# Performance work log

Measured on AMD Instinct MI355X. Metric: run time of the kernel, lower is better.

The kernel has to match this reference:

```python
import jax, jax.numpy as jnp
import numpy as np

LPB = 0.03   # lower_probability_bound
LEB = 0.2    # lower_entropy_bound
UEB = 0.5    # upper_entropy_bound
BETA = 1.0
N, K, S, D = 8192, 1000, 8, 1024


def setup_inputs() -> dict:
    key = jax.random.key(0)
    k1, k2, k3 = jax.random.split(key, 3)
    x = jax.random.normal(k1, (N, D), dtype=jnp.float32)
    # per-sample logit temperature so entropies spread across the gating band
    base = jax.random.normal(k2, (N, K), dtype=jnp.float32)
    scales = jax.random.uniform(k3, (N, 1), dtype=jnp.float32, minval=1.0, maxval=15.0)
    text_logits = base * scales
    memory = jnp.zeros((K, S, D), dtype=jnp.float32)
    # init_entropy(prop_max=1): -log(1/K) = log(K)
    memory_entropy = jnp.full((K, S), jnp.log(jnp.float32(K)), dtype=jnp.float32)
    memory_state = jnp.zeros((K, S), dtype=bool)
    return {"x": x, "text_logits": text_logits, "memory": memory,
            "memory_entropy": memory_entropy, "memory_state": memory_state}


def _update_memory(memory, memory_entropy, memory_state, x, text_logits):
    """Sequential entropy-gated scatter update (order-dependent, as in torch loop)."""
    def step(carry, inp):
        mem, ent, st = carry
        xi, li = inp                      # xi: [D], li: [K]
        p = jax.nn.softmax(li)
        lab = jnp.argmax(li)
        H = -jnp.sum(jnp.log(p + 1e-6) * p)  # shannon entropy
        row = ent[lab]                    # [S] entropies of this class's slots
        cond = (p[lab] > LPB) & (H > LEB) & (H < UEB) & jnp.any(H < row)
        idx = jnp.argmax(row)             # evict highest-entropy slot
        mem = mem.at[lab, idx].set(jnp.where(cond, xi, mem[lab, idx]))
        ent = ent.at[lab, idx].set(jnp.where(cond, H, ent[lab, idx]))
        st = st.at[lab, idx].set(jnp.where(cond, True, st[lab, idx]))
        return (mem, ent, st), cond

    (mem, ent, st), selected = jax.lax.scan(
        step, (memory, memory_entropy, memory_state), (x, text_logits))
    return mem, ent, st, selected


def reference(x, text_logits, memory, memory_entropy, memory_state):
    mem, ent, st, selected = _update_memory(memory, memory_entropy, memory_state, x, text_logits)
    # get_logits: A_ = (memory @ x.T).permute(2,0,1) -> [N, K, S]
    A_ = jnp.einsum('ksd,nd->nks', mem, x)
    logits = -jnp.sum(jnp.exp(-BETA * (1.0 - A_)), axis=-1)  # [N, K]
    return logits
```

## Files before the change

### kernel.cpp

```cpp
#include <hip/hip_runtime.h>
#include <hip/hip_bf16.h>
#include <math.h>

#define NN 8192
#define KK 1000
#define SS 8
#define DD 1024
#define RR (KK * SS)
#define RRP 8192

typedef __bf16 bf16x8 __attribute__((ext_vector_type(8)));
typedef float f32x4 __attribute__((ext_vector_type(4)));
typedef unsigned short ushort_t;
typedef ushort_t ushort8 __attribute__((ext_vector_type(8)));

static __device__ __forceinline__ ushort_t f2bf(float f) {
  unsigned u = __float_as_uint(f);
  unsigned r = (u + 0x7FFFu + ((u >> 16) & 1u)) >> 16;
  return (ushort_t)r;
}

#define GLD16(gsrc, ldst)                                                     \
  __builtin_amdgcn_global_load_lds(                                           \
      (const __attribute__((address_space(1))) unsigned int*)(gsrc),          \
      (__attribute__((address_space(3))) unsigned int*)(ldst), 16, 0, 0)

#define SBAR() asm volatile("s_barrier" ::: "memory")
#define WAITVM(n) asm volatile("s_waitcnt vmcnt(" #n ")" ::: "memory")

__global__ __launch_bounds__(256) void stats_kernel(
    const float* __restrict__ tl, int2* __restrict__ cand) {
  __shared__ float sv[KK];
  __shared__ float redv[256];
  __shared__ int   redi[256];
  const int n = blockIdx.x;
  const int t = threadIdx.x;
  const float* row = tl + (size_t)n * KK;
  for (int j = t; j < KK; j += 256) sv[j] = row[j];
  __syncthreads();

  float bv = -INFINITY; int bi = KK;
  for (int j = t; j < KK; j += 256) { float v = sv[j]; if (v > bv) { bv = v; bi = j; } }
  redv[t] = bv; redi[t] = bi;
  __syncthreads();
  for (int off = 128; off > 0; off >>= 1) {
    if (t < off) {
      float ov = redv[t + off]; int oi = redi[t + off];
      if (ov > redv[t] || (ov == redv[t] && oi < redi[t])) { redv[t] = ov; redi[t] = oi; }
    }
    __syncthreads();
  }
  const float m = redv[0];
  const int lab = redi[0];
  __syncthreads();

  float z = 0.f;
  for (int j = t; j < KK; j += 256) z += expf(sv[j] - m);
  redv[t] = z;
  __syncthreads();
  for (int off = 128; off > 0; off >>= 1) {
    if (t < off) redv[t] += redv[t + off];
    __syncthreads();
  }
  const float Z = redv[0];
  __syncthreads();

  float h = 0.f;
  for (int j = t; j < KK; j += 256) {
    float p = expf(sv[j] - m) / Z;
    h -= p * logf(p + 1e-6f);
  }
  redv[t] = h;
  __syncthreads();
  for (int off = 128; off > 0; off >>= 1) {
    if (t < off) redv[t] += redv[t + off];
    __syncthreads();
  }
  if (t == 0) {
    const float H = redv[0];
    const float plab = 1.0f / Z;
    const bool c = (plab > 0.03f) && (H > 0.2f) && (H < 0.5f);
    cand[n] = make_int2(c ? lab : -1, __float_as_int(H));
  }
}

__global__ __launch_bounds__(256) void select_kernel(
    const int2* __restrict__ cand, const float* __restrict__ ment,
    int* __restrict__ sel) {
  const int w = threadIdx.x >> 6;
  const int l = threadIdx.x & 63;
  const int k = blockIdx.x * 4 + w;
  if (k >= KK) return;

  float ent[SS]; int idx[SS];
  #pragma unroll
  for (int s = 0; s < SS; ++s) { ent[s] = ment[k * SS + s]; idx[s] = -1; }

  for (int base = 0; base < NN; base += 64) {
    const int2 c = cand[base + l];
    unsigned long long msk = __ballot(c.x == k);
    while (msk) {
      const int src = __ffsll((long long)msk) - 1;
      msk &= msk - 1;
      const float H = __shfl(__int_as_float(c.y), src);
      float mx = ent[0]; int mi = 0;
      #pragma unroll
      for (int s = 1; s < SS; ++s) if (ent[s] > mx) { mx = ent[s]; mi = s; }
      if (H < mx) { ent[mi] = H; idx[mi] = base + src; }
    }
  }
  if (l == 0) {
    #pragma unroll
    for (int s = 0; s < SS; ++s) sel[k * SS + s] = idx[s];
  }
}

__global__ __launch_bounds__(128) void convgather_kernel(
    const float* __restrict__ x, const float* __restrict__ mem,
    const int* __restrict__ sel, ushort_t* __restrict__ xb,
    ushort_t* __restrict__ Bb) {
  const int r = blockIdx.x;
  const int t = threadIdx.x;
  const float* src;
  ushort_t* dst;
  if (r < NN) {
    src = x + (size_t)r * DD;
    dst = xb + (size_t)r * DD;
  } else {
    const int rr = r - NN;
    dst = Bb + (size_t)rr * DD;
    if (rr >= RR) {
      *(ushort8*)(dst + t * 8) = (ushort8)0;
      return;
    }
    const int sl = sel[rr];
    src = (sl >= 0) ? (x + (size_t)sl * DD) : (mem + (size_t)rr * DD);
  }
  const float4 a = *(const float4*)(src + t * 8);
  const float4 b = *(const float4*)(src + t * 8 + 4);
  ushort8 o;
  o[0] = f2bf(a.x); o[1] = f2bf(a.y); o[2] = f2bf(a.z); o[3] = f2bf(a.w);
  o[4] = f2bf(b.x); o[5] = f2bf(b.y); o[6] = f2bf(b.z); o[7] = f2bf(b.w);
  *(ushort8*)(dst + t * 8) = o;
}

#define BKS 64
#define NTS (DD / BKS)
#define LDSH 32768

__global__ __launch_bounds__(512, 2) void logits_kernel(
    const ushort_t* __restrict__ xb, const ushort_t* __restrict__ Bb,
    float* __restrict__ out) {
  __shared__ ushort_t lds[2 * LDSH];
  const int t = threadIdx.x;
  const int w = t >> 6;
  const int l = t & 63;
  const int wm = w >> 2;
  const int wn = w & 3;
  const int n0 = blockIdx.x * 256;
  const int r0 = blockIdx.y * 256;

  const int srow = w * 8 + (l >> 3);
  const int gcolh = (((l & 7) ^ ((l >> 3) & 7)) << 3);
  const ushort_t* gA = xb + (size_t)(n0 + srow) * DD + gcolh;
  const ushort_t* gB = Bb + (size_t)(r0 + srow) * DD + gcolh;

#define STAGE_AC(T, c)                                                        \
  GLD16(gA + (size_t)(c) * 64 * DD + (size_t)(T) * BKS,                       \
        lds + ((T) & 1) * LDSH + (c) * 4096 + w * 512)
#define STAGE_BC(T, c)                                                        \
  GLD16(gB + (size_t)(c) * 64 * DD + (size_t)(T) * BKS,                       \
        lds + ((T) & 1) * LDSH + 16384 + (c) * 4096 + w * 512)

  const int lr = l & 15;
  const int ch = l >> 4;
  const int kc0 = ((ch ^ (lr & 7)) << 3);
  const int kc1 = (((4 + ch) ^ (lr & 7)) << 3);
  const int arow = (wm * 128 + lr) * 64;
  const int brow = 16384 + (wn * 64 + lr) * 64;

  f32x4 acc[8][4];
  #pragma unroll
  for (int mi = 0; mi < 8; ++mi)
    #pragma unroll
    for (int ni = 0; ni < 4; ++ni) acc[mi][ni] = (f32x4){0.f, 0.f, 0.f, 0.f};

  STAGE_AC(0, 0); STAGE_AC(0, 2);
  STAGE_BC(0, 0); STAGE_BC(0, 2);
  STAGE_BC(0, 1); STAGE_BC(0, 3);
  STAGE_AC(0, 1); STAGE_AC(0, 3);
  WAITVM(2);
  SBAR();

#define MFMA_CLUSTER(q)                                                       \
  do {                                                                        \
    __builtin_amdgcn_sched_barrier(0);                                        \
    __builtin_amdgcn_s_setprio(1);                                            \
    _Pragma("unroll")                                                         \
    for (int i = 0; i < 2; ++i)                                               \
      _Pragma("unroll")                                                       \
      for (int ni = 0; ni < 4; ++ni)                                          \
        acc[2 * (q) + i][ni] = __builtin_amdgcn_mfma_f32_16x16x32_bf16(       \
            af[i][0], bf[ni][0], acc[2 * (q) + i][ni], 0, 0, 0);              \
    _Pragma("unroll")                                                         \
    for (int i = 0; i < 2; ++i)                                               \
      _Pragma("unroll")                                                       \
      for (int ni = 0; ni < 4; ++ni)                                          \
        acc[2 * (q) + i][ni] = __builtin_amdgcn_mfma_f32_16x16x32_bf16(       \
            af[i][1], bf[ni][1], acc[2 * (q) + i][ni], 0, 0, 0);              \
    __builtin_amdgcn_s_setprio(0);                                            \
    __builtin_amdgcn_sched_barrier(0);                                        \
  } while (0)

  #pragma unroll 2
  for (int T = 0; T < NTS; ++T) {
    const ushort_t* buf = lds + (T & 1) * LDSH;
    const int Tn = T + 1;
    const bool st = (Tn < NTS);
    bf16x8 bf[4][2];
    bf16x8 af[2][2];

    #pragma unroll
    for (int ni = 0; ni < 4; ++ni) {
      bf[ni][0] = *(const bf16x8*)(buf + brow + ni * 1024 + kc0);
      bf[ni][1] = *(const bf16x8*)(buf + brow + ni * 1024 + kc1);
    }
    af[0][0] = *(const bf16x8*)(buf + arow + kc0);
    af[0][1] = *(const bf16x8*)(buf + arow + kc1);
    af[1][0] = *(const bf16x8*)(buf + arow + 1024 + kc0);
    af[1][1] = *(const bf16x8*)(buf + arow + 1024 + kc1);
    if (st) { STAGE_AC(Tn, 0); STAGE_AC(Tn, 2); }
    SBAR();
    MFMA_CLUSTER(0);
    SBAR();

    af[0][0] = *(const bf16x8*)(buf + arow + 2048 + kc0);
    af[0][1] = *(const bf16x8*)(buf + arow + 2048 + kc1);
    af[1][0] = *(const bf16x8*)(buf + arow + 3072 + kc0);
    af[1][1] = *(const bf16x8*)(buf + arow + 3072 + kc1);
    if (st) { STAGE_BC(Tn, 0); STAGE_BC(Tn, 2); }
    SBAR();
    MFMA_CLUSTER(1);
    SBAR();

    if (T < NTS - 1) { WAITVM(4); } else { WAITVM(0); }
    af[0][0] = *(const bf16x8*)(buf + arow + 4096 + kc0);
    af[0][1] = *(const bf16x8*)(buf + arow + 4096 + kc1);
    af[1][0] = *(const bf16x8*)(buf + arow + 5120 + kc0);
    af[1][1] = *(const bf16x8*)(buf + arow + 5120 + kc1);
    if (st) { STAGE_BC(Tn, 1); STAGE_BC(Tn, 3); }
    SBAR();
    MFMA_CLUSTER(2);
    SBAR();

    af[0][0] = *(const bf16x8*)(buf + arow + 6144 + kc0);
    af[0][1] = *(const bf16x8*)(buf + arow + 6144 + kc1);
    af[1][0] = *(const bf16x8*)(buf + arow + 7168 + kc0);
    af[1][1] = *(const bf16x8*)(buf + arow + 7168 + kc1);
    if (st) { STAGE_AC(Tn, 1); STAGE_AC(Tn, 3); }
    SBAR();
    MFMA_CLUSTER(3);
    WAITVM(2);
    SBAR();
  }

  const int rbase = n0 + wm * 128 + ((l >> 4) * 4);
  #pragma unroll
  for (int mi = 0; mi < 8; ++mi) {
    #pragma unroll
    for (int ni = 0; ni < 4; ++ni) {
      const int colbase = r0 + wn * 64 + ni * 16 + (l & 15);
      const int cls = colbase >> 3;
      #pragma unroll
      for (int rg = 0; rg < 4; ++rg) {
        float e = __expf(acc[mi][ni][rg] - 1.0f);
        e += __shfl_xor(e, 1);
        e += __shfl_xor(e, 2);
        e += __shfl_xor(e, 4);
        if ((l & 7) == 0 && cls < KK) {
          out[(size_t)(rbase + mi * 16 + rg) * KK + cls] = -fminf(e, 3.0e38f);
        }
      }
    }
  }
}

extern "C" void kernel_launch(void* const* d_in, const int* in_sizes, int n_in,
                              void* d_out, int out_size, void* d_ws, size_t ws_size,
                              hipStream_t stream) {
  const float* x    = (const float*)d_in[0];
  const float* tl   = (const float*)d_in[1];
  const float* mem  = (const float*)d_in[2];
  const float* ment = (const float*)d_in[3];
  float* out = (float*)d_out;

  char* ws = (char*)d_ws;
  int2*     cand = (int2*)ws;
  int*      sel  = (int*)(ws + NN * 8);
  ushort_t* Bb   = (ushort_t*)(ws + (1 << 20));
  ushort_t* xb   = (ushort_t*)(ws + (1 << 20) + (size_t)RRP * DD * 2);

  hipLaunchKernelGGL(stats_kernel, dim3(NN), dim3(256), 0, stream, tl, cand);
  hipLaunchKernelGGL(select_kernel, dim3(250), dim3(256), 0, stream, cand, ment, sel);
  hipLaunchKernelGGL(convgather_kernel, dim3(NN + RRP), dim3(128), 0, stream,
                     x, mem, sel, xb, Bb);
  hipLaunchKernelGGL(logits_kernel, dim3(32, 32), dim3(512), 0, stream, xb, Bb, out);
}
```

Before: 235.4 us.

## Quantize GEMM operands to FP8 and use scaled 16x16x128 MFMA

Converts x and the gathered memory rows to FP8 (e4m3) instead of bf16, halving operand bytes. The logits GEMM now uses the scaled f8f6f4 MFMA with K=128 per instruction, doubling the K per tile and cutting the number of MFMA and LDS instructions. The intent is to double matrix throughput and halve memory traffic. The cost is much lower precision in dot products of length 1024, and exp(A-1) amplifies errors in large A values, so accuracy against the reference may fail.

```diff
diff --git a/kernel.cpp b/kernel.cpp
--- a/kernel.cpp
+++ b/kernel.cpp
@@ -9,16 +9,10 @@
 #define RR (KK * SS)
 #define RRP 8192
 
-typedef __bf16 bf16x8 __attribute__((ext_vector_type(8)));
 typedef float f32x4 __attribute__((ext_vector_type(4)));
-typedef unsigned short ushort_t;
-typedef ushort_t ushort8 __attribute__((ext_vector_type(8)));
-
-static __device__ __forceinline__ ushort_t f2bf(float f) {
-  unsigned u = __float_as_uint(f);
-  unsigned r = (u + 0x7FFFu + ((u >> 16) & 1u)) >> 16;
-  return (ushort_t)r;
-}
+typedef int i32x4 __attribute__((ext_vector_type(4)));
+typedef int i32x8 __attribute__((ext_vector_type(8)));
+typedef unsigned char u8;
 
 #define GLD16(gsrc, ldst)                                                     \
   __builtin_amdgcn_global_load_lds(                                           \
@@ -117,20 +111,19 @@
 
 __global__ __launch_bounds__(128) void convgather_kernel(
     const float* __restrict__ x, const float* __restrict__ mem,
-    const int* __restrict__ sel, ushort_t* __restrict__ xb,
-    ushort_t* __restrict__ Bb) {
+    const int* __restrict__ sel, u8* __restrict__ xq, u8* __restrict__ Bq) {
   const int r = blockIdx.x;
   const int t = threadIdx.x;
   const float* src;
-  ushort_t* dst;
+  u8* dst;
   if (r < NN) {
     src = x + (size_t)r * DD;
-    dst = xb + (size_t)r * DD;
+    dst = xq + (size_t)r * DD;
   } else {
     const int rr = r - NN;
-    dst = Bb + (size_t)rr * DD;
+    dst = Bq + (size_t)rr * DD;
     if (rr >= RR) {
-      *(ushort8*)(dst + t * 8) = (ushort8)0;
+      *(int2*)(dst + t * 8) = make_int2(0, 0);
       return;
     }
     const int sl = sel[rr];
@@ -138,20 +131,21 @@
   }
   const float4 a = *(const float4*)(src + t * 8);
   const float4 b = *(const float4*)(src + t * 8 + 4);
-  ushort8 o;
-  o[0] = f2bf(a.x); o[1] = f2bf(a.y); o[2] = f2bf(a.z); o[3] = f2bf(a.w);
-  o[4] = f2bf(b.x); o[5] = f2bf(b.y); o[6] = f2bf(b.z); o[7] = f2bf(b.w);
-  *(ushort8*)(dst + t * 8) = o;
-}
-
-#define BKS 64
-#define NTS (DD / BKS)
-#define LDSH 32768
+  int lo = __builtin_amdgcn_cvt_pk_fp8_f32(a.x, a.y, 0, false);
+  lo = __builtin_amdgcn_cvt_pk_fp8_f32(a.z, a.w, lo, true);
+  int hi = __builtin_amdgcn_cvt_pk_fp8_f32(b.x, b.y, 0, false);
+  hi = __builtin_amdgcn_cvt_pk_fp8_f32(b.z, b.w, hi, true);
+  *(int2*)(dst + t * 8) = make_int2(lo, hi);
+}
+
+#define BKQ 128
+#define NTS (DD / BKQ)
+#define LDSB 65536
 
 __global__ __launch_bounds__(512, 2) void logits_kernel(
-    const ushort_t* __restrict__ xb, const ushort_t* __restrict__ Bb,
+    const u8* __restrict__ xq, const u8* __restrict__ Bq,
     float* __restrict__ out) {
-  __shared__ ushort_t lds[2 * LDSH];
+  __shared__ u8 lds[2 * LDSB];
   const int t = threadIdx.x;
   const int w = t >> 6;
   const int l = t & 63;
@@ -161,23 +155,23 @@
   const int r0 = blockIdx.y * 256;
 
   const int srow = w * 8 + (l >> 3);
-  const int gcolh = (((l & 7) ^ ((l >> 3) & 7)) << 3);
-  const ushort_t* gA = xb + (size_t)(n0 + srow) * DD + gcolh;
-  const ushort_t* gB = Bb + (size_t)(r0 + srow) * DD + gcolh;
+  const int gcolb = (((l & 7) ^ ((l >> 3) & 7)) << 4);
+  const u8* gA = xq + (size_t)(n0 + srow) * DD + gcolb;
+  const u8* gB = Bq + (size_t)(r0 + srow) * DD + gcolb;
 
 #define STAGE_AC(T, c)                                                        \
-  GLD16(gA + (size_t)(c) * 64 * DD + (size_t)(T) * BKS,                       \
-        lds + ((T) & 1) * LDSH + (c) * 4096 + w * 512)
+  GLD16(gA + (size_t)(c) * 64 * DD + (size_t)(T) * BKQ,                       \
+        lds + ((T) & 1) * LDSB + (c) * 8192 + w * 1024)
 #define STAGE_BC(T, c)                                                        \
-  GLD16(gB + (size_t)(c) * 64 * DD + (size_t)(T) * BKS,                       \
-        lds + ((T) & 1) * LDSH + 16384 + (c) * 4096 + w * 512)
+  GLD16(gB + (size_t)(c) * 64 * DD + (size_t)(T) * BKQ,                       \
+        lds + ((T) & 1) * LDSB + 32768 + (c) * 8192 + w * 1024)
 
   const int lr = l & 15;
-  const int ch = l >> 4;
-  const int kc0 = ((ch ^ (lr & 7)) << 3);
-  const int kc1 = (((4 + ch) ^ (lr & 7)) << 3);
-  const int arow = (wm * 128 + lr) * 64;
-  const int brow = 16384 + (wn * 64 + lr) * 64;
+  const int g = l >> 4;
+  const int kc0 = (((g * 2) ^ (lr & 7)) << 4);
+  const int kc1 = (((g * 2 + 1) ^ (lr & 7)) << 4);
+  const int arow = (wm * 128 + lr) * 128;
+  const int brow = 32768 + (wn * 64 + lr) * 128;
 
   f32x4 acc[8][4];
   #pragma unroll
@@ -191,6 +185,11 @@
   STAGE_AC(0, 1); STAGE_AC(0, 3);
   WAITVM(2);
   SBAR();
+
+#define LDSFRAG(base)                                                         \
+  __builtin_shufflevector(*(const i32x4*)(bufc + (base) + kc0),               \
+                          *(const i32x4*)(bufc + (base) + kc1),               \
+                          0, 1, 2, 3, 4, 5, 6, 7)
 
 #define MFMA_CLUSTER(q)                                                       \
   do {                                                                        \
@@ -200,63 +199,48 @@
     for (int i = 0; i < 2; ++i)                                               \
       _Pragma("unroll")                                                       \
       for (int ni = 0; ni < 4; ++ni)                                          \
-        acc[2 * (q) + i][ni] = __builtin_amdgcn_mfma_f32_16x16x32_bf16(       \
-            af[i][0], bf[ni][0], acc[2 * (q) + i][ni], 0, 0, 0);              \
-    _Pragma("unroll")                                                         \
-    for (int i = 0; i < 2; ++i)                                               \
-      _Pragma("unroll")                                                       \
-      for (int ni = 0; ni < 4; ++ni)                                          \
-        acc[2 * (q) + i][ni] = __builtin_amdgcn_mfma_f32_16x16x32_bf16(       \
-            af[i][1], bf[ni][1], acc[2 * (q) + i][ni], 0, 0, 0);              \
+        acc[2 * (q) + i][ni] =                                                \
+            __builtin_amdgcn_mfma_scale_f32_16x16x128_f8f6f4(                 \
+                af[i], bf[ni], acc[2 * (q) + i][ni], 0, 0,                    \
+                0, 0x7F7F7F7F, 0, 0x7F7F7F7F);                                \
     __builtin_amdgcn_s_setprio(0);                                            \
     __builtin_amdgcn_sched_barrier(0);                                        \
   } while (0)
 
   #pragma unroll 2
   for (int T = 0; T < NTS; ++T) {
-    const ushort_t* buf = lds + (T & 1) * LDSH;
+    const u8* bufc = lds + (T & 1) * LDSB;
     const int Tn = T + 1;
     const bool st = (Tn < NTS);
-    bf16x8 bf[4][2];
-    bf16x8 af[2][2];
-
-    #pragma unroll
-    for (int ni = 0; ni < 4; ++ni) {
-      bf[ni][0] = *(const bf16x8*)(buf + brow + ni * 1024 + kc0);
-      bf[ni][1] = *(const bf16x8*)(buf + brow + ni * 1024 + kc1);
-    }
-    af[0][0] = *(const bf16x8*)(buf + arow + kc0);
-    af[0][1] = *(const bf16x8*)(buf + arow + kc1);
-    af[1][0] = *(const bf16x8*)(buf + arow + 1024 + kc0);
-    af[1][1] = *(const bf16x8*)(buf + arow + 1024 + kc1);
+    i32x8 bf[4];
+    i32x8 af[2];
+
+    #pragma unroll
+    for (int ni = 0; ni < 4; ++ni) bf[ni] = LDSFRAG(brow + ni * 2048);
+    af[0] = LDSFRAG(arow);
+    af[1] = LDSFRAG(arow + 2048);
     if (st) { STAGE_AC(Tn, 0); STAGE_AC(Tn, 2); }
     SBAR();
     MFMA_CLUSTER(0);
     SBAR();
 
-    af[0][0] = *(const bf16x8*)(buf + arow + 2048 + kc0);
-    af[0][1] = *(const bf16x8*)(buf + arow + 2048 + kc1);
-    af[1][0] = *(const bf16x8*)(buf + arow + 3072 + kc0);
-    af[1][1] = *(const bf16x8*)(buf + arow + 3072 + kc1);
+    af[0] = LDSFRAG(arow + 4096);
+    af[1] = LDSFRAG(arow + 6144);
     if (st) { STAGE_BC(Tn, 0); STAGE_BC(Tn, 2); }
     SBAR();
     MFMA_CLUSTER(1);
     SBAR();
 
     if (T < NTS - 1) { WAITVM(4); } else { WAITVM(0); }
-    af[0][0] = *(const bf16x8*)(buf + arow + 4096 + kc0);
-    af[0][1] = *(const bf16x8*)(buf + arow + 4096 + kc1);
-    af[1][0] = *(const bf16x8*)(buf + arow + 5120 + kc0);
-    af[1][1] = *(const bf16x8*)(buf + arow + 5120 + kc1);
+    af[0] = LDSFRAG(arow + 8192);
+    af[1] = LDSFRAG(arow + 10240);
     if (st) { STAGE_BC(Tn, 1); STAGE_BC(Tn, 3); }
     SBAR();
     MFMA_CLUSTER(2);
     SBAR();
 
-    af[0][0] = *(const bf16x8*)(buf + arow + 6144 + kc0);
-    af[0][1] = *(const bf16x8*)(buf + arow + 6144 + kc1);
-    af[1][0] = *(const bf16x8*)(buf + arow + 7168 + kc0);
-    af[1][1] = *(const bf16x8*)(buf + arow + 7168 + kc1);
+    af[0] = LDSFRAG(arow + 12288);
+    af[1] = LDSFRAG(arow + 14336);
     if (st) { STAGE_AC(Tn, 1); STAGE_AC(Tn, 3); }
     SBAR();
     MFMA_CLUSTER(3);
@@ -295,14 +279,14 @@
   float* out = (float*)d_out;
 
   char* ws = (char*)d_ws;
-  int2*     cand = (int2*)ws;
-  int*      sel  = (int*)(ws + NN * 8);
-  ushort_t* Bb   = (ushort_t*)(ws + (1 << 20));
-  ushort_t* xb   = (ushort_t*)(ws + (1 << 20) + (size_t)RRP * DD * 2);
+  int2* cand = (int2*)ws;
+  int*  sel  = (int*)(ws + NN * 8);
+  u8*   Bq   = (u8*)(ws + (1 << 20));
+  u8*   xq   = (u8*)(ws + (1 << 20) + (size_t)RRP * DD);
 
   hipLaunchKernelGGL(stats_kernel, dim3(NN), dim3(256), 0, stream, tl, cand);
   hipLaunchKernelGGL(select_kernel, dim3(250), dim3(256), 0, stream, cand, ment, sel);
   hipLaunchKernelGGL(convgather_kernel, dim3(NN + RRP), dim3(128), 0, stream,
-                     x, mem, sel, xb, Bb);
-  hipLaunchKernelGGL(logits_kernel, dim3(32, 32), dim3(512), 0, stream, xb, Bb, out);
-}
+                     x, mem, sel, xq, Bq);
+  hipLaunchKernelGGL(logits_kernel, dim3(32, 32), dim3(512), 0, stream, xq, Bq, out);
+}
```

Result: slower. 399.4 us (+69.7%).
